# Performance work log

Hardware: AMD Instinct MI355X
Metric: run time of the kernel (lower is better)

The kernel has to match this reference:

```python
import jax, jax.numpy as jnp
import numpy as np

ESL, B, EHS, DHS = 4096, 64, 256, 256

def setup_inputs() -> dict:
    key = jax.random.key(0)
    k1, k2, k3 = jax.random.split(key, 3)
    si_1 = jax.random.normal(k1, (1, B, DHS), dtype=jnp.float32)
    h = jax.random.normal(k2, (ESL, B, EHS), dtype=jnp.float32)
    # nn.Linear(ehs+dhs, 1): weight [1, ehs+dhs], bias [1]
    W = jax.random.normal(k3, (1, EHS + DHS), dtype=jnp.float32) * (1.0 / np.sqrt(EHS + DHS))
    b = jnp.zeros((1,), dtype=jnp.float32)
    return {"si_1": si_1, "h": h, "W": W, "b": b}

def reference(si_1, h, W, b):
    # cat((si_1.repeat(esl,1,1), h), dim=2) @ W.T == si_1 @ Wd.T + h @ We.T
    # (first dhs columns of W act on si_1, remaining ehs on h)
    dhs = si_1.shape[-1]
    Wd, We = W[:, :dhs], W[:, dhs:]              # [1, dhs], [1, ehs]
    e_dec = jnp.einsum('obd,kd->obk', si_1, Wd)   # [1, B, 1]
    e_enc = jnp.einsum('sbe,ke->sbk', h, We)      # [S, B, 1]
    energy = jax.nn.relu(e_dec + e_enc + b)       # [S, B, 1]
    attention = jax.nn.softmax(energy, axis=0)    # softmax over seq dim
    # einsum('snk,snl->knl', attention, h) -> [1, B, EHS]
    context = jnp.einsum('snk,snl->knl', attention, h)
    return context
```

## Files before the change

kernel.cpp:

```cpp
#include <hip/hip_runtime.h>
#include <math.h>

constexpr int ESL = 4096;
constexpr int B   = 64;
constexpr int EHS = 256;
constexpr int DHS = 256;

constexpr int NC    = 32;
constexpr int CHUNK = ESL / NC;
constexpr int TPB   = 256;
constexpr int WAVES = TPB / 64;
constexpr int SPW   = CHUNK / WAVES;

__device__ __forceinline__ float wave_sum(float v) {
#pragma unroll
  for (int off = 32; off > 0; off >>= 1)
    v += __shfl_xor(v, off, 64);
  return v;
}

__global__ __launch_bounds__(TPB) void pass1(
    const float* __restrict__ si, const float* __restrict__ h,
    const float* __restrict__ W,  const float* __restrict__ bptr,
    float* __restrict__ ws_acc, float* __restrict__ ws_m, float* __restrict__ ws_l) {
  const int c    = blockIdx.x;
  const int n    = blockIdx.y;
  const int lane = threadIdx.x & 63;
  const int w    = threadIdx.x >> 6;

  const float4 Wd4 = *(const float4*)(W + 4 * lane);
  const float4 We4 = *(const float4*)(W + DHS + 4 * lane);
  const float  bias = bptr[0];

  const float4 si4 = *(const float4*)(si + (size_t)n * DHS + 4 * lane);
  const float edec = wave_sum(si4.x * Wd4.x + si4.y * Wd4.y +
                              si4.z * Wd4.z + si4.w * Wd4.w) + bias;

  float  m = -1e30f, l = 0.f;
  float4 acc = make_float4(0.f, 0.f, 0.f, 0.f);

  const int    s0     = c * CHUNK + w;
  const float* hp     = h + ((size_t)s0 * B + n) * EHS + 4 * lane;
  const size_t stride = (size_t)WAVES * B * EHS;

  float4 h4 = *(const float4*)hp;
#pragma unroll 4
  for (int t = 0; t < SPW; ++t) {
    float4 h4n = make_float4(0.f, 0.f, 0.f, 0.f);
    if (t + 1 < SPW) h4n = *(const float4*)(hp + (size_t)(t + 1) * stride);

    float p = h4.x * We4.x + h4.y * We4.y + h4.z * We4.z + h4.w * We4.w;
    float e = wave_sum(p) + edec;
    e = fmaxf(e, 0.f);

    float mn  = fmaxf(m, e);
    float sc  = __expf(m - mn);
    float wgt = __expf(e - mn);
    l = l * sc + wgt;
    acc.x = acc.x * sc + wgt * h4.x;
    acc.y = acc.y * sc + wgt * h4.y;
    acc.z = acc.z * sc + wgt * h4.z;
    acc.w = acc.w * sc + wgt * h4.w;
    m = mn;
    h4 = h4n;
  }

  __shared__ float sm_m[WAVES], sm_l[WAVES];
  __shared__ float sm_acc[WAVES][EHS];
  if (lane == 0) { sm_m[w] = m; sm_l[w] = l; }
  *(float4*)&sm_acc[w][4 * lane] = acc;
  __syncthreads();

  const int j = threadIdx.x;
  float M = fmaxf(fmaxf(sm_m[0], sm_m[1]), fmaxf(sm_m[2], sm_m[3]));
  float L = 0.f, A = 0.f;
#pragma unroll
  for (int ww = 0; ww < WAVES; ++ww) {
    float scw = __expf(sm_m[ww] - M);
    L += sm_l[ww] * scw;
    A += sm_acc[ww][j] * scw;
  }
  const size_t pidx = (size_t)n * NC + c;
  ws_acc[pidx * EHS + j] = A;
  if (j == 0) { ws_m[pidx] = M; ws_l[pidx] = L; }
}

__global__ __launch_bounds__(EHS) void pass2(
    const float* __restrict__ ws_acc, const float* __restrict__ ws_m,
    const float* __restrict__ ws_l, float* __restrict__ out) {
  const int n = blockIdx.x;
  const int j = threadIdx.x;

  float M = -1e30f;
#pragma unroll
  for (int c = 0; c < NC; ++c) M = fmaxf(M, ws_m[(size_t)n * NC + c]);

  float L = 0.f, A = 0.f;
#pragma unroll
  for (int c = 0; c < NC; ++c) {
    const size_t pidx = (size_t)n * NC + c;
    float sc = __expf(ws_m[pidx] - M);
    L += ws_l[pidx] * sc;
    A += ws_acc[pidx * EHS + j] * sc;
  }
  out[(size_t)n * EHS + j] = A / L;
}

extern "C" void kernel_launch(void* const* d_in, const int* in_sizes, int n_in,
                              void* d_out, int out_size, void* d_ws, size_t ws_size,
                              hipStream_t stream) {
  const float* si   = (const float*)d_in[0];
  const float* h    = (const float*)d_in[1];
  const float* W    = (const float*)d_in[2];
  const float* bptr = (const float*)d_in[3];
  float* out = (float*)d_out;

  float* ws_acc = (float*)d_ws;
  float* ws_m   = ws_acc + (size_t)B * NC * EHS;
  float* ws_l   = ws_m + (size_t)B * NC;

  dim3 g1(NC, B);
  pass1<<<g1, TPB, 0, stream>>>(si, h, W, bptr, ws_acc, ws_m, ws_l);
  pass2<<<B, EHS, 0, stream>>>(ws_acc, ws_m, ws_l, out);
}
```

Before: 371.9 us.

## Drop running-max softmax and reduce two sequence rows per wave shuffle pass

Removes online-softmax max tracking and rescaling in both passes, using plain exp(e) with additive partial sums. This drops the ws_m buffer and the per-step rescale exps. Each wave now processes two sequence rows per iteration: a single xor-32 exchange combines the halves, then one 5-step shuffle reduction serves both rows, and the weights are broadcast with readlane. This shortens the serial shuffle/exp dependency chain per row, at the cost of possible exp overflow for large energies.

```diff
diff --git a/kernel.cpp b/kernel.cpp
--- a/kernel.cpp
+++ b/kernel.cpp
@@ -11,98 +11,107 @@
 constexpr int TPB   = 256;
 constexpr int WAVES = TPB / 64;
 constexpr int SPW   = CHUNK / WAVES;
+constexpr int PAIRS = SPW / 2;
 
-__device__ __forceinline__ float wave_sum(float v) {
+__device__ __forceinline__ float wave_sum64(float v) {
 #pragma unroll
   for (int off = 32; off > 0; off >>= 1)
     v += __shfl_xor(v, off, 64);
   return v;
 }
 
+__device__ __forceinline__ float bcast_lane(float v, int lane) {
+  return __uint_as_float(__builtin_amdgcn_readlane(__float_as_uint(v), lane));
+}
+
 __global__ __launch_bounds__(TPB) void pass1(
     const float* __restrict__ si, const float* __restrict__ h,
     const float* __restrict__ W,  const float* __restrict__ bptr,
-    float* __restrict__ ws_acc, float* __restrict__ ws_m, float* __restrict__ ws_l) {
+    float* __restrict__ ws_acc, float* __restrict__ ws_l) {
   const int c    = blockIdx.x;
   const int n    = blockIdx.y;
   const int lane = threadIdx.x & 63;
   const int w    = threadIdx.x >> 6;
 
-  const float4 Wd4 = *(const float4*)(W + 4 * lane);
-  const float4 We4 = *(const float4*)(W + DHS + 4 * lane);
+  const float4 Wd4  = *(const float4*)(W + 4 * lane);
+  const float4 We4  = *(const float4*)(W + DHS + 4 * lane);
   const float  bias = bptr[0];
 
   const float4 si4 = *(const float4*)(si + (size_t)n * DHS + 4 * lane);
-  const float edec = wave_sum(si4.x * Wd4.x + si4.y * Wd4.y +
-                              si4.z * Wd4.z + si4.w * Wd4.w) + bias;
+  const float edec = wave_sum64(si4.x * Wd4.x + si4.y * Wd4.y +
+                                si4.z * Wd4.z + si4.w * Wd4.w) + bias;
 
-  float  m = -1e30f, l = 0.f;
+  const size_t rowstride = (size_t)B * EHS;
+  const float* hp = h + ((size_t)(c * CHUNK + w) * B + n) * EHS + 4 * lane;
+
+  float  l   = 0.f;
   float4 acc = make_float4(0.f, 0.f, 0.f, 0.f);
 
-  const int    s0     = c * CHUNK + w;
-  const float* hp     = h + ((size_t)s0 * B + n) * EHS + 4 * lane;
-  const size_t stride = (size_t)WAVES * B * EHS;
+  float4 a4 = *(const float4*)hp;
+  float4 b4 = *(const float4*)(hp + (size_t)WAVES * rowstride);
 
-  float4 h4 = *(const float4*)hp;
 #pragma unroll 4
-  for (int t = 0; t < SPW; ++t) {
-    float4 h4n = make_float4(0.f, 0.f, 0.f, 0.f);
-    if (t + 1 < SPW) h4n = *(const float4*)(hp + (size_t)(t + 1) * stride);
+  for (int u = 0; u < PAIRS; ++u) {
+    float4 a4n = make_float4(0.f, 0.f, 0.f, 0.f);
+    float4 b4n = a4n;
+    if (u + 1 < PAIRS) {
+      const float* p = hp + (size_t)(u + 1) * (2 * WAVES) * rowstride;
+      a4n = *(const float4*)p;
+      b4n = *(const float4*)(p + (size_t)WAVES * rowstride);
+    }
 
-    float p = h4.x * We4.x + h4.y * We4.y + h4.z * We4.z + h4.w * We4.w;
-    float e = wave_sum(p) + edec;
-    e = fmaxf(e, 0.f);
+    float p0 = a4.x * We4.x + a4.y * We4.y + a4.z * We4.z + a4.w * We4.w;
+    float p1 = b4.x * We4.x + b4.y * We4.y + b4.z * We4.z + b4.w * We4.w;
 
-    float mn  = fmaxf(m, e);
-    float sc  = __expf(m - mn);
-    float wgt = __expf(e - mn);
-    l = l * sc + wgt;
-    acc.x = acc.x * sc + wgt * h4.x;
-    acc.y = acc.y * sc + wgt * h4.y;
-    acc.z = acc.z * sc + wgt * h4.z;
-    acc.w = acc.w * sc + wgt * h4.w;
-    m = mn;
-    h4 = h4n;
+    float t0 = p0 + __shfl_xor(p0, 32, 64);
+    float t1 = p1 + __shfl_xor(p1, 32, 64);
+    float cc = (lane < 32) ? t0 : t1;
+#pragma unroll
+    for (int off = 16; off > 0; off >>= 1)
+      cc += __shfl_xor(cc, off, 64);
+
+    float e  = fmaxf(cc + edec, 0.f);
+    float wv = __expf(e);
+    float w0 = bcast_lane(wv, 0);
+    float w1 = bcast_lane(wv, 32);
+
+    l += w0 + w1;
+    acc.x += w0 * a4.x + w1 * b4.x;
+    acc.y += w0 * a4.y + w1 * b4.y;
+    acc.z += w0 * a4.z + w1 * b4.z;
+    acc.w += w0 * a4.w + w1 * b4.w;
+
+    a4 = a4n; b4 = b4n;
   }
 
-  __shared__ float sm_m[WAVES], sm_l[WAVES];
   __shared__ float sm_acc[WAVES][EHS];
-  if (lane == 0) { sm_m[w] = m; sm_l[w] = l; }
+  __shared__ float sm_l[WAVES];
   *(float4*)&sm_acc[w][4 * lane] = acc;
+  if (lane == 0) sm_l[w] = l;
   __syncthreads();
 
   const int j = threadIdx.x;
-  float M = fmaxf(fmaxf(sm_m[0], sm_m[1]), fmaxf(sm_m[2], sm_m[3]));
-  float L = 0.f, A = 0.f;
-#pragma unroll
-  for (int ww = 0; ww < WAVES; ++ww) {
-    float scw = __expf(sm_m[ww] - M);
-    L += sm_l[ww] * scw;
-    A += sm_acc[ww][j] * scw;
-  }
+  float A = sm_acc[0][j] + sm_acc[1][j] + sm_acc[2][j] + sm_acc[3][j];
   const size_t pidx = (size_t)n * NC + c;
   ws_acc[pidx * EHS + j] = A;
-  if (j == 0) { ws_m[pidx] = M; ws_l[pidx] = L; }
+  if (j == 0) ws_l[pidx] = sm_l[0] + sm_l[1] + sm_l[2] + sm_l[3];
 }
 
 __global__ __launch_bounds__(EHS) void pass2(
-    const float* __restrict__ ws_acc, const float* __restrict__ ws_m,
-    const float* __restrict__ ws_l, float* __restrict__ out) {
+    const float* __restrict__ ws_acc, const float* __restrict__ ws_l,
+    float* __restrict__ out) {
   const int n = blockIdx.x;
   const int j = threadIdx.x;
 
-  float M = -1e30f;
+  float L = 0.f;
 #pragma unroll
-  for (int c = 0; c < NC; ++c) M = fmaxf(M, ws_m[(size_t)n * NC + c]);
+  for (int c = 0; c < NC; ++c) L += ws_l[(size_t)n * NC + c];
 
-  float L = 0.f, A = 0.f;
+  float A = 0.f;
 #pragma unroll
-  for (int c = 0; c < NC; ++c) {
-    const size_t pidx = (size_t)n * NC + c;
-    float sc = __expf(ws_m[pidx] - M);
-    L += ws_l[pidx] * sc;
-    A += ws_acc[pidx * EHS + j] * sc;
-  }
+  for (int c = 0; c < NC; ++c)
+    A += ws_acc[((size_t)n * NC + c) * EHS + j];
+
   out[(size_t)n * EHS + j] = A / L;
 }
 
@@ -116,10 +125,9 @@
   float* out = (float*)d_out;
 
   float* ws_acc = (float*)d_ws;
-  float* ws_m   = ws_acc + (size_t)B * NC * EHS;
-  float* ws_l   = ws_m + (size_t)B * NC;
+  float* ws_l   = ws_acc + (size_t)B * NC * EHS;
 
   dim3 g1(NC, B);
-  pass1<<<g1, TPB, 0, stream>>>(si, h, W, bptr, ws_acc, ws_m, ws_l);
-  pass2<<<B, EHS, 0, stream>>>(ws_acc, ws_m, ws_l, out);
+  pass1<<<g1, TPB, 0, stream>>>(si, h, W, bptr, ws_acc, ws_l);
+  pass2<<<B, EHS, 0, stream>>>(ws_acc, ws_l, out);
 }
```

Result: slower. 384.9 us (+3.5%).
